# Kernel tuning notes

Measured on AMD Instinct MI355X. Metric: run time of the kernel, lower is better.

## Reference

```python
import jax, jax.numpy as jnp
import numpy as np

N = 4096
IN_F = 512
OUT_F = 64
HEADS = 4
ALPHA = 0.2  # leaky relu slope
NEG_INF = -9e15


def setup_inputs() -> dict:
    key = jax.random.key(0)
    k1, k2, k3, k4 = jax.random.split(key, 4)
    x = jax.random.normal(k1, (N, IN_F), dtype=jnp.float32)
    adj = jax.random.randint(k2, (N, N), 0, 2, dtype=jnp.int32)
    # xavier-uniform-like init for params
    limW = float(np.sqrt(6.0 / (IN_F + OUT_F * HEADS)))
    W = jax.random.uniform(k3, (IN_F, OUT_F * HEADS), dtype=jnp.float32, minval=-limW, maxval=limW)
    lima = float(np.sqrt(6.0 / (2 * OUT_F + 1)))
    a = jax.random.uniform(k4, (2 * OUT_F, 1), dtype=jnp.float32, minval=-lima, maxval=lima)
    return {"x": x, "adj": adj, "W": W, "a": a}


def reference(x, adj, W, a):
    # h: [N, H, F]
    h = (x @ W).reshape(N, HEADS, OUT_F)
    a_src = a[:OUT_F, 0]   # [F]
    a_dst = a[OUT_F:, 0]   # [F]
    s = jnp.einsum("nhf,f->nh", h, a_src)  # source-node score [N, H]
    t = jnp.einsum("nhf,f->nh", h, a_dst)  # dest-node score   [N, H]
    # e[i, j, k] = leaky_relu(s[i,k] + t[j,k]) -> [N, N, H]
    e = jax.nn.leaky_relu(s[:, None, :] + t[None, :, :], negative_slope=ALPHA)
    mask = (adj > 0)[:, :, None]  # [N, N, 1]
    e = jnp.where(mask, e, NEG_INF)
    attn = jax.nn.softmax(e, axis=1)  # softmax over neighbors j
    # weighted aggregation per head: [N, H, F]
    h_prime = jnp.einsum("ijh,jhf->ihf", attn, h)
    return h_prime.reshape(N, HEADS * OUT_F)
```

## Files before the change

kernel.cpp:

```cpp
#include <hip/hip_runtime.h>
#include <hip/hip_bf16.h>


#define NN 4096
#define KF 512
#define NF 256

typedef __attribute__((ext_vector_type(8))) short bf16x8;
typedef __attribute__((ext_vector_type(4))) short s16x4;
typedef __attribute__((ext_vector_type(4))) float f32x4;

union AB8 { bf16x8 v; short2 h[4]; short s[8]; int4 i4; };
union ST4 { s16x4 v; short2 h[2]; };
union I64 { long v; int i[2]; };

__device__ __forceinline__ short f2bf(float f) {
    union { float f; unsigned u; } v; v.f = f;
    unsigned r = v.u + 0x7fffu + ((v.u >> 16) & 1u);
    return (short)(r >> 16);
}
__device__ __forceinline__ short2 pkbf(float a, float b) {
    __hip_bfloat162 t = __float22bfloat162_rn(make_float2(a, b));
    union { __hip_bfloat162 v; short2 s; } u; u.v = t;
    return u.s;
}
__device__ __forceinline__ int pkfp8x4(float a, float b, float c, float d) {
    int p = __builtin_amdgcn_cvt_pk_fp8_f32(a, b, 0, false);
    p     = __builtin_amdgcn_cvt_pk_fp8_f32(c, d, p, true);
    return p;
}

__global__ __launch_bounds__(256) void stage1(const float* __restrict__ x,
                                              const float* __restrict__ W,
                                              short* __restrict__ xF,
                                              short* __restrict__ WtF) {
    if (blockIdx.x < 1024) {
        const int lane = threadIdx.x & 63, wv = threadIdx.x >> 6;
        const int i = blockIdx.x * 4 + wv;
        const float4* xp = (const float4*)(x + (size_t)i * KF + lane * 8);
        float4 xa = xp[0], xb = xp[1];
        ST4 o0, o1;
        o0.h[0] = pkbf(xa.x, xa.y); o0.h[1] = pkbf(xa.z, xa.w);
        o1.h[0] = pkbf(xb.x, xb.y); o1.h[1] = pkbf(xb.z, xb.w);
        const int kblk = lane >> 2, qk = lane & 3;
        const int jgrp = i >> 4, r = i & 15;
        short* dst = xF + ((size_t)(kblk * 256 + jgrp) * 64 + qk * 16 + r) * 8;
        *(s16x4*)dst = o0.v;
        *(s16x4*)(dst + 4) = o1.v;
    } else {
        int tid = (blockIdx.x - 1024) * 256 + threadIdx.x;
        int l = tid & 63, nt = (tid >> 6) & 3, hd = (tid >> 8) & 3, kblk = tid >> 10;
        int q = l >> 4, r = l & 15;
        int col = hd * 64 + nt * 16 + r;
        int k0 = kblk * 32 + q * 8;
        AB8 o;
        #pragma unroll
        for (int e = 0; e < 8; e++) o.s[e] = f2bf(W[(k0 + e) * NF + col]);
        *(bf16x8*)(WtF + (size_t)tid * 8) = o.v;
    }
}

__global__ __launch_bounds__(256) void stage2(const short* __restrict__ xF,
                                              const short* __restrict__ WtF,
                                              const float* __restrict__ a,
                                              const int* __restrict__ adj,
                                              unsigned char* __restrict__ VtF8,
                                              float* __restrict__ ipk,
                                              float2* __restrict__ jpk,
                                              unsigned* __restrict__ pT) {
    if (blockIdx.x < 256) {
        const int lane = threadIdx.x & 63, wv = threadIdx.x >> 6;
        const int q = lane >> 4, r = lane & 15;
        const int jb32 = blockIdx.x >> 1, ch = blockIdx.x & 1;
        const int rg = wv >> 1, hd = ch * 2 + (wv & 1);
        const int jgrp = jb32 * 2 + rg;

        const short* ap = xF  + ((size_t)jgrp * 64 + lane) * 8;
        const short* wp = WtF + ((size_t)(hd * 4) * 64 + lane) * 8;

        f32x4 acc[4] = {};
        #pragma unroll
        for (int kblk = 0; kblk < 16; kblk++) {
            bf16x8 av = *(const bf16x8*)(ap + (size_t)kblk * 256 * 512);
            const short* w = wp + (size_t)kblk * 16 * 512;
            #pragma unroll
            for (int nt = 0; nt < 4; nt++) {
                bf16x8 bv = *(const bf16x8*)(w + nt * 512);
                acc[nt] = __builtin_amdgcn_mfma_f32_16x16x32_bf16(av, bv, acc[nt], 0, 0, 0);
            }
        }
        const int base = rg * 16 + q * 4;
        const int qa = base >> 3, e0 = base & 7;
        #pragma unroll
        for (int nt = 0; nt < 4; nt++) {
            size_t slot = (size_t)(((jb32 * 4 + hd) * 4 + nt) * 64 + qa * 16 + r);
            *(int*)(VtF8 + slot * 8 + e0) = pkfp8x4(acc[nt][0], acc[nt][1], acc[nt][2], acc[nt][3]);
        }
        float as[4], at[4];
        #pragma unroll
        for (int nt = 0; nt < 4; nt++) { as[nt] = a[nt * 16 + r]; at[nt] = a[64 + nt * 16 + r]; }
        f32x4 sp = {}, tp = {};
        #pragma unroll
        for (int nt = 0; nt < 4; nt++)
            #pragma unroll
            for (int reg = 0; reg < 4; reg++) {
                sp[reg] += acc[nt][reg] * as[nt];
                tp[reg] += acc[nt][reg] * at[nt];
            }
        #pragma unroll
        for (int d = 1; d < 16; d <<= 1)
            #pragma unroll
            for (int reg = 0; reg < 4; reg++) {
                sp[reg] += __shfl_xor(sp[reg], d, 64);
                tp[reg] += __shfl_xor(tp[reg], d, 64);
            }
        if (r == 0) {
            #pragma unroll
            for (int reg = 0; reg < 4; reg++) {
                int j = jb32 * 32 + rg * 16 + q * 4 + reg;
                ipk[hd * NN + j] = __expf(-0.8f * sp[reg]);
                jpk[hd * NN + j] = make_float2(__expf(tp[reg]), __expf(0.2f * tp[reg]));
            }
        }
    } else {
        int gw   = ((blockIdx.x - 256) * 256 + threadIdx.x) >> 6;
        int lane = threadIdx.x & 63;
        int i = gw >> 4, seg = gw & 15;
        const int* ap = adj + (size_t)i * NN + seg * 256 + lane;
        unsigned long long b0 = __ballot(ap[0]   != 0);
        unsigned long long b1 = __ballot(ap[64]  != 0);
        unsigned long long b2 = __ballot(ap[128] != 0);
        unsigned long long b3 = __ballot(ap[192] != 0);
        if (lane == 0) {
            *(uint4*)(pT + ((size_t)(seg * 2    ) * NN + i) * 4) =
                make_uint4((unsigned)b0, (unsigned)(b0 >> 32), (unsigned)b1, (unsigned)(b1 >> 32));
            *(uint4*)(pT + ((size_t)(seg * 2 + 1) * NN + i) * 4) =
                make_uint4((unsigned)b2, (unsigned)(b2 >> 32), (unsigned)b3, (unsigned)(b3 >> 32));
        }
    }
}

__global__ __launch_bounds__(512, 4)
void gat_attn(const uint4* __restrict__ pT4, const float* __restrict__ ipk,
              const float* __restrict__ jpkf, const unsigned char* __restrict__ VtF8,
              float* __restrict__ out) {
    const int lane = threadIdx.x & 63, js = threadIdx.x >> 6;
    const int hd = blockIdx.x & 3, it32 = blockIdx.x >> 2;
    const int q = lane >> 4, r = lane & 15;
    const int i0 = it32 * 32, ia = i0 + r;
    const float cia = ipk[hd * NN + ia];
    const float cib = ipk[hd * NN + ia + 16];
    const int qs = q * 8;

    __shared__ unsigned lut[16];
    __shared__ float sacc[7][10][64][4];
    if (threadIdx.x < 16) {
        unsigned m01 = (threadIdx.x * 0x204081u) & 0x01010101u;
        lut[threadIdx.x] = m01 * 0xFFu;
    }
    __syncthreads();

    f32x4 acc[10] = {};
    const long ones = 0x3838383838383838L;

    const int it0 = js * 16;
    const float* jp = jpkf + (size_t)hd * NN * 2 + 2 * ((it0 << 5) + qs);
    const long*  vp = (const long*)(VtF8 + (size_t)(it0 * 16 + hd * 4) * 512) + lane;
    const uint4* prow = pT4 + (size_t)(js * 4) * NN + ia;

    auto iset = [&](unsigned w, float ci, f32x4* ac,
                    float4 ja, float4 jb, float4 jc, float4 jd,
                    long v0, long v1, long v2, long v3) {
        float p0 = fmaxf(ja.x, ci * ja.y);
        float p1 = fmaxf(ja.z, ci * ja.w);
        float p2 = fmaxf(jb.x, ci * jb.y);
        float p3 = fmaxf(jb.z, ci * jb.w);
        float p4 = fmaxf(jc.x, ci * jc.y);
        float p5 = fmaxf(jc.z, ci * jc.w);
        float p6 = fmaxf(jd.x, ci * jd.y);
        float p7 = fmaxf(jd.z, ci * jd.w);
        I64 af;
        af.i[0] = pkfp8x4(p0, p1, p2, p3) & (int)lut[w & 15u];
        af.i[1] = pkfp8x4(p4, p5, p6, p7) & (int)lut[(w >> 4) & 15u];
        ac[0] = __builtin_amdgcn_mfma_f32_16x16x32_fp8_fp8(af.v, v0, ac[0], 0, 0, 0);
        ac[1] = __builtin_amdgcn_mfma_f32_16x16x32_fp8_fp8(af.v, v1, ac[1], 0, 0, 0);
        ac[2] = __builtin_amdgcn_mfma_f32_16x16x32_fp8_fp8(af.v, v2, ac[2], 0, 0, 0);
        ac[3] = __builtin_amdgcn_mfma_f32_16x16x32_fp8_fp8(af.v, v3, ac[3], 0, 0, 0);
        ac[4] = __builtin_amdgcn_mfma_f32_16x16x32_fp8_fp8(af.v, ones, ac[4], 0, 0, 0);
    };

    #pragma unroll 1
    for (int g = 0; g < 4; g++) {
        uint4 wga = prow[(size_t)g * NN];
        uint4 wgb = prow[(size_t)g * NN + 16];
        #pragma unroll
        for (int u = 0; u < 4; u++) {
            unsigned wa = (u == 0 ? wga.x : u == 1 ? wga.y : u == 2 ? wga.z : wga.w) >> qs;
            unsigned wb = (u == 0 ? wgb.x : u == 1 ? wgb.y : u == 2 ? wgb.z : wgb.w) >> qs;
            const float4* jpv = (const float4*)jp;
            float4 ja = jpv[0], jb = jpv[1], jc = jpv[2], jd = jpv[3];
            long v0 = vp[0], v1 = vp[64], v2 = vp[128], v3 = vp[192];
            iset(wa, cia, acc,     ja, jb, jc, jd, v0, v1, v2, v3);
            iset(wb, cib, acc + 5, ja, jb, jc, jd, v0, v1, v2, v3);
            jp += 64; vp += 1024;
        }
    }

    if (js > 0) {
        #pragma unroll
        for (int t = 0; t < 10; t++)
            *(f32x4*)&sacc[js - 1][t][lane][0] = acc[t];
    }
    __syncthreads();
    if (js == 0) {
        #pragma unroll 1
        for (int gg = 0; gg < 7; gg++)
            #pragma unroll
            for (int t = 0; t < 10; t++) {
                f32x4 o = *(const f32x4*)&sacc[gg][t][lane][0];
                acc[t][0] += o[0]; acc[t][1] += o[1];
                acc[t][2] += o[2]; acc[t][3] += o[3];
            }
        #pragma unroll
        for (int reg = 0; reg < 4; reg++) {
            float inva = 1.f / acc[4][reg];
            float invb = 1.f / acc[9][reg];
            int rowa = i0 + q * 4 + reg;
            #pragma unroll
            for (int t = 0; t < 4; t++) {
                out[(size_t)rowa * NF + hd * 64 + t * 16 + r] = acc[t][reg] * inva;
                out[(size_t)(rowa + 16) * NF + hd * 64 + t * 16 + r] = acc[t + 5][reg] * invb;
            }
        }
    }
}

extern "C" void kernel_launch(void* const* d_in, const int* in_sizes, int n_in,
                              void* d_out, int out_size, void* d_ws, size_t ws_size,
                              hipStream_t stream) {
    const float* x   = (const float*)d_in[0];
    const int*   adj = (const int*)d_in[1];
    const float* W   = (const float*)d_in[2];
    const float* a   = (const float*)d_in[3];
    float* out = (float*)d_out;

    char* ws = (char*)d_ws;
    short*         xF   = (short*)ws;
    short*         WtF  = (short*)(ws + 4194304);
    unsigned char* VtF8 = (unsigned char*)(ws + 4456448);
    unsigned*      pT   = (unsigned*)(ws + 5505024);
    float*         ipk  = (float*)(ws + 7602176);
    float2*        jpk  = (float2*)(ws + 7667712);

    stage1  <<<1088, 256, 0, stream>>>(x, W, xF, WtF);
    stage2  <<<16640, 256, 0, stream>>>(xF, WtF, a, adj, VtF8, ipk, jpk, pT);
    gat_attn<<<512, 512, 0, stream>>>((const uint4*)pT, ipk, (const float*)jpk, VtF8, out);
}
```

Measured before the change: 127.9 us.

## Fuse bf16 conversion into projection GEMM and widen attention blocks to 1024 threads

Removes the separate stage1 kernel that converted x and W to bf16 in MFMA-friendly layouts. The projection kernel now reads fp32 x and W directly and converts them in registers, which saves a launch and a workspace round trip but uses strided, uncoalesced W loads that each block repeats. The attention kernel now handles 64 rows per block with 1024 threads and a two-level shared-memory tree reduction, halving the number of blocks.

```diff
diff --git a/kernel.cpp b/kernel.cpp
--- a/kernel.cpp
+++ b/kernel.cpp
@@ -30,38 +30,8 @@
     return p;
 }
 
-__global__ __launch_bounds__(256) void stage1(const float* __restrict__ x,
+__global__ __launch_bounds__(256) void stage2(const float* __restrict__ x,
                                               const float* __restrict__ W,
-                                              short* __restrict__ xF,
-                                              short* __restrict__ WtF) {
-    if (blockIdx.x < 1024) {
-        const int lane = threadIdx.x & 63, wv = threadIdx.x >> 6;
-        const int i = blockIdx.x * 4 + wv;
-        const float4* xp = (const float4*)(x + (size_t)i * KF + lane * 8);
-        float4 xa = xp[0], xb = xp[1];
-        ST4 o0, o1;
-        o0.h[0] = pkbf(xa.x, xa.y); o0.h[1] = pkbf(xa.z, xa.w);
-        o1.h[0] = pkbf(xb.x, xb.y); o1.h[1] = pkbf(xb.z, xb.w);
-        const int kblk = lane >> 2, qk = lane & 3;
-        const int jgrp = i >> 4, r = i & 15;
-        short* dst = xF + ((size_t)(kblk * 256 + jgrp) * 64 + qk * 16 + r) * 8;
-        *(s16x4*)dst = o0.v;
-        *(s16x4*)(dst + 4) = o1.v;
-    } else {
-        int tid = (blockIdx.x - 1024) * 256 + threadIdx.x;
-        int l = tid & 63, nt = (tid >> 6) & 3, hd = (tid >> 8) & 3, kblk = tid >> 10;
-        int q = l >> 4, r = l & 15;
-        int col = hd * 64 + nt * 16 + r;
-        int k0 = kblk * 32 + q * 8;
-        AB8 o;
-        #pragma unroll
-        for (int e = 0; e < 8; e++) o.s[e] = f2bf(W[(k0 + e) * NF + col]);
-        *(bf16x8*)(WtF + (size_t)tid * 8) = o.v;
-    }
-}
-
-__global__ __launch_bounds__(256) void stage2(const short* __restrict__ xF,
-                                              const short* __restrict__ WtF,
                                               const float* __restrict__ a,
                                               const int* __restrict__ adj,
                                               unsigned char* __restrict__ VtF8,
@@ -75,18 +45,24 @@
         const int rg = wv >> 1, hd = ch * 2 + (wv & 1);
         const int jgrp = jb32 * 2 + rg;
 
-        const short* ap = xF  + ((size_t)jgrp * 64 + lane) * 8;
-        const short* wp = WtF + ((size_t)(hd * 4) * 64 + lane) * 8;
+        const float* xp = x + (size_t)(jgrp * 16 + r) * KF + q * 8;
+        const float* wp = W + hd * 64 + r;
 
         f32x4 acc[4] = {};
-        #pragma unroll
+        #pragma unroll 2
         for (int kblk = 0; kblk < 16; kblk++) {
-            bf16x8 av = *(const bf16x8*)(ap + (size_t)kblk * 256 * 512);
-            const short* w = wp + (size_t)kblk * 16 * 512;
+            float4 xa = *(const float4*)(xp + kblk * 32);
+            float4 xb = *(const float4*)(xp + kblk * 32 + 4);
+            AB8 av;
+            av.h[0] = pkbf(xa.x, xa.y);  av.h[1] = pkbf(xa.z, xa.w);
+            av.h[2] = pkbf(xb.x, xb.y);  av.h[3] = pkbf(xb.z, xb.w);
+            const float* wk = wp + (size_t)(kblk * 32 + q * 8) * NF;
             #pragma unroll
             for (int nt = 0; nt < 4; nt++) {
-                bf16x8 bv = *(const bf16x8*)(w + nt * 512);
-                acc[nt] = __builtin_amdgcn_mfma_f32_16x16x32_bf16(av, bv, acc[nt], 0, 0, 0);
+                AB8 bv;
+                #pragma unroll
+                for (int e = 0; e < 8; e++) bv.s[e] = f2bf(wk[e * NF + nt * 16]);
+                acc[nt] = __builtin_amdgcn_mfma_f32_16x16x32_bf16(av.v, bv.v, acc[nt], 0, 0, 0);
             }
         }
         const int base = rg * 16 + q * 4;
@@ -140,20 +116,21 @@
     }
 }
 
-__global__ __launch_bounds__(512, 4)
+__global__ __launch_bounds__(1024, 4)
 void gat_attn(const uint4* __restrict__ pT4, const float* __restrict__ ipk,
               const float* __restrict__ jpkf, const unsigned char* __restrict__ VtF8,
               float* __restrict__ out) {
-    const int lane = threadIdx.x & 63, js = threadIdx.x >> 6;
-    const int hd = blockIdx.x & 3, it32 = blockIdx.x >> 2;
+    const int lane = threadIdx.x & 63, wv = threadIdx.x >> 6;
+    const int js = wv & 7, ih = wv >> 3;
+    const int hd = blockIdx.x & 3, it64 = blockIdx.x >> 2;
     const int q = lane >> 4, r = lane & 15;
-    const int i0 = it32 * 32, ia = i0 + r;
+    const int i0 = it64 * 64 + ih * 32, ia = i0 + r;
     const float cia = ipk[hd * NN + ia];
     const float cib = ipk[hd * NN + ia + 16];
     const int qs = q * 8;
 
     __shared__ unsigned lut[16];
-    __shared__ float sacc[7][10][64][4];
+    __shared__ float sacc[2][4][10][64][4];
     if (threadIdx.x < 16) {
         unsigned m01 = (threadIdx.x * 0x204081u) & 0x01010101u;
         lut[threadIdx.x] = m01 * 0xFFu;
@@ -206,18 +183,33 @@
         }
     }
 
-    if (js > 0) {
+    if (js >= 4) {
         #pragma unroll
         for (int t = 0; t < 10; t++)
-            *(f32x4*)&sacc[js - 1][t][lane][0] = acc[t];
+            *(f32x4*)&sacc[ih][js - 4][t][lane][0] = acc[t];
+    }
+    __syncthreads();
+    if (js < 4) {
+        #pragma unroll
+        for (int t = 0; t < 10; t++) {
+            f32x4 o = *(const f32x4*)&sacc[ih][js][t][lane][0];
+            acc[t][0] += o[0]; acc[t][1] += o[1];
+            acc[t][2] += o[2]; acc[t][3] += o[3];
+        }
+    }
+    __syncthreads();
+    if (js >= 1 && js < 4) {
+        #pragma unroll
+        for (int t = 0; t < 10; t++)
+            *(f32x4*)&sacc[ih][js - 1][t][lane][0] = acc[t];
     }
     __syncthreads();
     if (js == 0) {
         #pragma unroll 1
-        for (int gg = 0; gg < 7; gg++)
+        for (int gg = 0; gg < 3; gg++)
             #pragma unroll
             for (int t = 0; t < 10; t++) {
-                f32x4 o = *(const f32x4*)&sacc[gg][t][lane][0];
+                f32x4 o = *(const f32x4*)&sacc[ih][gg][t][lane][0];
                 acc[t][0] += o[0]; acc[t][1] += o[1];
                 acc[t][2] += o[2]; acc[t][3] += o[3];
             }
@@ -245,14 +237,11 @@
     float* out = (float*)d_out;
 
     char* ws = (char*)d_ws;
-    short*         xF   = (short*)ws;
-    short*         WtF  = (short*)(ws + 4194304);
-    unsigned char* VtF8 = (unsigned char*)(ws + 4456448);
-    unsigned*      pT   = (unsigned*)(ws + 5505024);
-    float*         ipk  = (float*)(ws + 7602176);
-    float2*        jpk  = (float2*)(ws + 7667712);
-
-    stage1  <<<1088, 256, 0, stream>>>(x, W, xF, WtF);
-    stage2  <<<16640, 256, 0, stream>>>(xF, WtF, a, adj, VtF8, ipk, jpk, pT);
-    gat_attn<<<512, 512, 0, stream>>>((const uint4*)pT, ipk, (const float*)jpk, VtF8, out);
-}
+    unsigned char* VtF8 = (unsigned char*)ws;
+    unsigned*      pT   = (unsigned*)(ws + 1048576);
+    float*         ipk  = (float*)(ws + 3145728);
+    float2*        jpk  = (float2*)(ws + 3211264);
+
+    stage2  <<<16640, 256, 0, stream>>>(x, W, a, adj, VtF8, ipk, jpk, pT);
+    gat_attn<<<256, 1024, 0, stream>>>((const uint4*)pT, ipk, (const float*)jpk, VtF8, out);
+}
```

New measurement: 133.7 us. 1.05x slower.

## Interleave fp8 V layout for 16-byte loads, tree-reduce partials, raise occupancy

Applied to the files above, without the earlier changes.

Stage1 now writes the fp8 V tiles so that the four column tiles for each lane sit next to each other. The attention kernel can then fetch them with two 16-byte loads instead of four scattered 8-byte loads. The cross-wave reduction becomes a two-level tree, which shrinks shared memory for partial sums from seven slots to four. Launch bounds move to a minimum of 6 blocks per CU, which may cost registers or cause spills in exchange for the extra occupancy.

```diff
diff --git a/kernel.cpp b/kernel.cpp
--- a/kernel.cpp
+++ b/kernel.cpp
@@ -13,6 +13,7 @@
 union AB8 { bf16x8 v; short2 h[4]; short s[8]; int4 i4; };
 union ST4 { s16x4 v; short2 h[2]; };
 union I64 { long v; int i[2]; };
+union V16 { int4 q; long l[2]; };
 
 __device__ __forceinline__ short f2bf(float f) {
     union { float f; unsigned u; } v; v.f = f;
@@ -93,8 +94,8 @@
         const int qa = base >> 3, e0 = base & 7;
         #pragma unroll
         for (int nt = 0; nt < 4; nt++) {
-            size_t slot = (size_t)(((jb32 * 4 + hd) * 4 + nt) * 64 + qa * 16 + r);
-            *(int*)(VtF8 + slot * 8 + e0) = pkfp8x4(acc[nt][0], acc[nt][1], acc[nt][2], acc[nt][3]);
+            size_t addr = ((size_t)((jb32 * 4 + hd) * 64 + qa * 16 + r) * 4 + nt) * 8 + e0;
+            *(int*)(VtF8 + addr) = pkfp8x4(acc[nt][0], acc[nt][1], acc[nt][2], acc[nt][3]);
         }
         float as[4], at[4];
         #pragma unroll
@@ -140,7 +141,7 @@
     }
 }
 
-__global__ __launch_bounds__(512, 4)
+__global__ __launch_bounds__(512, 6)
 void gat_attn(const uint4* __restrict__ pT4, const float* __restrict__ ipk,
               const float* __restrict__ jpkf, const unsigned char* __restrict__ VtF8,
               float* __restrict__ out) {
@@ -153,7 +154,7 @@
     const int qs = q * 8;
 
     __shared__ unsigned lut[16];
-    __shared__ float sacc[7][10][64][4];
+    __shared__ float sacc[4][10][64][4];
     if (threadIdx.x < 16) {
         unsigned m01 = (threadIdx.x * 0x204081u) & 0x01010101u;
         lut[threadIdx.x] = m01 * 0xFFu;
@@ -165,7 +166,7 @@
 
     const int it0 = js * 16;
     const float* jp = jpkf + (size_t)hd * NN * 2 + 2 * ((it0 << 5) + qs);
-    const long*  vp = (const long*)(VtF8 + (size_t)(it0 * 16 + hd * 4) * 512) + lane;
+    const int4*  vq = (const int4*)(VtF8 + ((size_t)(it0 * 4 + hd) * 64 + lane) * 32);
     const uint4* prow = pT4 + (size_t)(js * 4) * NN + ia;
 
     auto iset = [&](unsigned w, float ci, f32x4* ac,
@@ -199,14 +200,29 @@
             unsigned wb = (u == 0 ? wgb.x : u == 1 ? wgb.y : u == 2 ? wgb.z : wgb.w) >> qs;
             const float4* jpv = (const float4*)jp;
             float4 ja = jpv[0], jb = jpv[1], jc = jpv[2], jd = jpv[3];
-            long v0 = vp[0], v1 = vp[64], v2 = vp[128], v3 = vp[192];
-            iset(wa, cia, acc,     ja, jb, jc, jd, v0, v1, v2, v3);
-            iset(wb, cib, acc + 5, ja, jb, jc, jd, v0, v1, v2, v3);
-            jp += 64; vp += 1024;
-        }
-    }
-
-    if (js > 0) {
+            V16 va, vb; va.q = vq[0]; vb.q = vq[1];
+            iset(wa, cia, acc,     ja, jb, jc, jd, va.l[0], va.l[1], vb.l[0], vb.l[1]);
+            iset(wb, cib, acc + 5, ja, jb, jc, jd, va.l[0], va.l[1], vb.l[0], vb.l[1]);
+            jp += 64; vq += 512;
+        }
+    }
+
+    if (js >= 4) {
+        #pragma unroll
+        for (int t = 0; t < 10; t++)
+            *(f32x4*)&sacc[js - 4][t][lane][0] = acc[t];
+    }
+    __syncthreads();
+    if (js < 4) {
+        #pragma unroll
+        for (int t = 0; t < 10; t++) {
+            f32x4 o = *(const f32x4*)&sacc[js][t][lane][0];
+            acc[t][0] += o[0]; acc[t][1] += o[1];
+            acc[t][2] += o[2]; acc[t][3] += o[3];
+        }
+    }
+    __syncthreads();
+    if (js >= 1 && js < 4) {
         #pragma unroll
         for (int t = 0; t < 10; t++)
             *(f32x4*)&sacc[js - 1][t][lane][0] = acc[t];
@@ -214,7 +230,7 @@
     __syncthreads();
     if (js == 0) {
         #pragma unroll 1
-        for (int gg = 0; gg < 7; gg++)
+        for (int gg = 0; gg < 3; gg++)
             #pragma unroll
             for (int t = 0; t < 10; t++) {
                 f32x4 o = *(const f32x4*)&sacc[gg][t][lane][0];
```

New measurement: 159.4 us. +24.7%, slower.

## Interleave fp8 V tiles per lane, compute byte masks inline, and preload adjacency words

Applied to the files above, without the earlier changes.

Changes the fp8 V layout written by the projection stage so each lane's four n-tile 8-byte fragments sit contiguously. The attention kernel can then fetch them with two 16-byte loads instead of four strided 8-byte loads. It also drops the shared-memory mask LUT and its barrier in favour of an arithmetic byte-mask, and hoists all adjacency bitmask loads ahead of the main loop. This cuts load instruction count and LDS lookups at the cost of a few extra ALU ops and more live registers, which could affect occupancy.

```diff
diff --git a/kernel.cpp b/kernel.cpp
--- a/kernel.cpp
+++ b/kernel.cpp
@@ -13,6 +13,7 @@
 union AB8 { bf16x8 v; short2 h[4]; short s[8]; int4 i4; };
 union ST4 { s16x4 v; short2 h[2]; };
 union I64 { long v; int i[2]; };
+union V16 { int4 q; long l[2]; };
 
 __device__ __forceinline__ short f2bf(float f) {
     union { float f; unsigned u; } v; v.f = f;
@@ -28,6 +29,9 @@
     int p = __builtin_amdgcn_cvt_pk_fp8_f32(a, b, 0, false);
     p     = __builtin_amdgcn_cvt_pk_fp8_f32(c, d, p, true);
     return p;
+}
+__device__ __forceinline__ int bytemask(unsigned n) {
+    return (int)(((n * 0x204081u) & 0x01010101u) * 0xFFu);
 }
 
 __global__ __launch_bounds__(256) void stage1(const float* __restrict__ x,
@@ -93,8 +97,8 @@
         const int qa = base >> 3, e0 = base & 7;
         #pragma unroll
         for (int nt = 0; nt < 4; nt++) {
-            size_t slot = (size_t)(((jb32 * 4 + hd) * 4 + nt) * 64 + qa * 16 + r);
-            *(int*)(VtF8 + slot * 8 + e0) = pkfp8x4(acc[nt][0], acc[nt][1], acc[nt][2], acc[nt][3]);
+            size_t addr = ((size_t)((jb32 * 4 + hd) * 64 + qa * 16 + r) * 4 + nt) * 8 + e0;
+            *(int*)(VtF8 + addr) = pkfp8x4(acc[nt][0], acc[nt][1], acc[nt][2], acc[nt][3]);
         }
         float as[4], at[4];
         #pragma unroll
@@ -152,21 +156,22 @@
     const float cib = ipk[hd * NN + ia + 16];
     const int qs = q * 8;
 
-    __shared__ unsigned lut[16];
     __shared__ float sacc[7][10][64][4];
-    if (threadIdx.x < 16) {
-        unsigned m01 = (threadIdx.x * 0x204081u) & 0x01010101u;
-        lut[threadIdx.x] = m01 * 0xFFu;
-    }
-    __syncthreads();
 
     f32x4 acc[10] = {};
     const long ones = 0x3838383838383838L;
 
     const int it0 = js * 16;
     const float* jp = jpkf + (size_t)hd * NN * 2 + 2 * ((it0 << 5) + qs);
-    const long*  vp = (const long*)(VtF8 + (size_t)(it0 * 16 + hd * 4) * 512) + lane;
+    const int4*  vq = (const int4*)(VtF8 + ((size_t)(it0 * 4 + hd) * 64 + lane) * 32);
     const uint4* prow = pT4 + (size_t)(js * 4) * NN + ia;
+
+    uint4 WA[4], WB[4];
+    #pragma unroll
+    for (int g = 0; g < 4; g++) {
+        WA[g] = prow[(size_t)g * NN];
+        WB[g] = prow[(size_t)g * NN + 16];
+    }
 
     auto iset = [&](unsigned w, float ci, f32x4* ac,
                     float4 ja, float4 jb, float4 jc, float4 jd,
@@ -180,8 +185,8 @@
         float p6 = fmaxf(jd.x, ci * jd.y);
         float p7 = fmaxf(jd.z, ci * jd.w);
         I64 af;
-        af.i[0] = pkfp8x4(p0, p1, p2, p3) & (int)lut[w & 15u];
-        af.i[1] = pkfp8x4(p4, p5, p6, p7) & (int)lut[(w >> 4) & 15u];
+        af.i[0] = pkfp8x4(p0, p1, p2, p3) & bytemask(w & 15u);
+        af.i[1] = pkfp8x4(p4, p5, p6, p7) & bytemask((w >> 4) & 15u);
         ac[0] = __builtin_amdgcn_mfma_f32_16x16x32_fp8_fp8(af.v, v0, ac[0], 0, 0, 0);
         ac[1] = __builtin_amdgcn_mfma_f32_16x16x32_fp8_fp8(af.v, v1, ac[1], 0, 0, 0);
         ac[2] = __builtin_amdgcn_mfma_f32_16x16x32_fp8_fp8(af.v, v2, ac[2], 0, 0, 0);
@@ -191,18 +196,17 @@
 
     #pragma unroll 1
     for (int g = 0; g < 4; g++) {
-        uint4 wga = prow[(size_t)g * NN];
-        uint4 wgb = prow[(size_t)g * NN + 16];
+        uint4 wga = WA[g], wgb = WB[g];
         #pragma unroll
         for (int u = 0; u < 4; u++) {
             unsigned wa = (u == 0 ? wga.x : u == 1 ? wga.y : u == 2 ? wga.z : wga.w) >> qs;
             unsigned wb = (u == 0 ? wgb.x : u == 1 ? wgb.y : u == 2 ? wgb.z : wgb.w) >> qs;
             const float4* jpv = (const float4*)jp;
             float4 ja = jpv[0], jb = jpv[1], jc = jpv[2], jd = jpv[3];
-            long v0 = vp[0], v1 = vp[64], v2 = vp[128], v3 = vp[192];
-            iset(wa, cia, acc,     ja, jb, jc, jd, v0, v1, v2, v3);
-            iset(wb, cib, acc + 5, ja, jb, jc, jd, v0, v1, v2, v3);
-            jp += 64; vp += 1024;
+            V16 va, vb; va.q = vq[0]; vb.q = vq[1];
+            iset(wa, cia, acc,     ja, jb, jc, jd, va.l[0], va.l[1], vb.l[0], vb.l[1]);
+            iset(wb, cib, acc + 5, ja, jb, jc, jd, va.l[0], va.l[1], vb.l[0], vb.l[1]);
+            jp += 64; vq += 512;
         }
     }
 
```

New measurement: 143.6 us. 1.12x slower.
